# Kernel tuning notes

Hardware: AMD Instinct MI355X
Metric: run time of the kernel (lower is better)

Reference implementation:

```python
import jax, jax.numpy as jnp
import numpy as np

T, HW, C = 64, 24, 1024
MID = 256
WIN = 2  # 'video' forward_type -> 2x2 windows


def setup_inputs() -> dict:
    key = jax.random.key(0)
    k1, k2, k3, k4, k5 = jax.random.split(key, 5)
    return {
        "image_features": jax.random.normal(k1, (T, HW * HW, C), dtype=jnp.float32),
        "Wq": jax.random.normal(k2, (C, MID), dtype=jnp.float32) * 0.02,
        "bq": jax.random.normal(k3, (MID,), dtype=jnp.float32) * 0.02,
        "Wk": jax.random.normal(k4, (C, MID), dtype=jnp.float32) * 0.02,
        "bk": jax.random.normal(k5, (MID,), dtype=jnp.float32) * 0.02,
    }


def reference(image_features, Wq, bq, Wk, bk):
    # forward_type == 'video': 2x2 windowed attention over pooled patches
    t, n, c = image_features.shape
    H = W = int(np.sqrt(n))
    h2, w2 = H // WIN, W // WIN
    # [T, H, W, C] -> [T, h2, 2, w2, 2, C] -> [T, h2, w2, 2, 2, C] -> [T, P, 4, C]
    x = image_features.reshape(t, h2, WIN, w2, WIN, c)
    windows = x.transpose(0, 1, 3, 2, 4, 5).reshape(t, h2 * w2, WIN * WIN, c)
    # avg_pool2d(2,2) == mean over each 2x2 window
    pooled = windows.mean(axis=2)  # [T, P, C]
    q = pooled @ Wq + bq           # [T, P, MID]
    k = windows @ Wk + bk          # [T, P, 4, MID]
    scale = 1.0 / jnp.sqrt(jnp.float32(MID))
    attn = jnp.einsum("tpd,tpwd->tpw", q, k) * scale  # [T, P, 4]
    attn = jnp.nan_to_num(attn)
    attn = jax.nn.softmax(attn, axis=-1)
    attn_feat = jnp.einsum("tpw,tpwc->tpc", attn, windows)  # softmax-weighted value avg
    # query dim has size 1, so .mean(1) in torch is identity here
    return pooled + attn_feat  # [T, P, C]; new_image_size = (h2, w2) is static
```

## Files before the change

kernel.cpp:

```cpp
#include <hip/hip_runtime.h>

#define T_ 64
#define P_ 144
#define NPAIR 9216
#define C_ 1024
#define MID_ 256

typedef __attribute__((ext_vector_type(4))) float f32x4;
typedef __attribute__((ext_vector_type(8))) __bf16 bf16x8;
typedef __attribute__((ext_vector_type(4))) __bf16 bf16x4;

__device__ __forceinline__ void async_copy16(const void* g, void* l) {
  __builtin_amdgcn_global_load_lds(
      (const __attribute__((address_space(1))) unsigned int*)g,
      (__attribute__((address_space(3))) unsigned int*)l, 16, 0, 0);
}

__global__ __launch_bounds__(256) void pool_prep_kernel(
    const float* __restrict__ img, const float* __restrict__ Wq,
    const float* __restrict__ Wk, __bf16* __restrict__ poolb,
    __bf16* __restrict__ Wqt, __bf16* __restrict__ Wkb) {
  const int bid = blockIdx.x;
  const int tid = threadIdx.x;
  if (bid < NPAIR) {
    const int t = bid / P_;
    const int p = bid - t * P_;
    const int wy = p / 12, wx = p - wy * 12;
    const int c = tid * 4;
    const float* base = img + ((size_t)t * 576 + 48 * wy + 2 * wx) * C_;
    f32x4 s = *(const f32x4*)(base + c);
    s += *(const f32x4*)(base + (size_t)1 * C_ + c);
    s += *(const f32x4*)(base + (size_t)24 * C_ + c);
    s += *(const f32x4*)(base + (size_t)25 * C_ + c);
    s *= 0.25f;
    bf16x4 pv;
#pragma unroll
    for (int j = 0; j < 4; ++j) pv[j] = (__bf16)s[j];
    *(bf16x4*)(poolb + (size_t)bid * C_ + c) = pv;
  } else if (bid < NPAIR + 64) {
    const int b = bid - NPAIR;
    const int ct = b >> 3, dt = b & 7;
    __shared__ float tile[128][33];
    const int r = tid >> 3;
    const int c4 = (tid & 7) * 4;
#pragma unroll
    for (int s = 0; s < 4; ++s) {
      const int row = r + s * 32;
      const f32x4 v =
          *(const f32x4*)(Wq + (size_t)(ct * 128 + row) * MID_ + dt * 32 + c4);
      tile[row][c4 + 0] = v[0]; tile[row][c4 + 1] = v[1];
      tile[row][c4 + 2] = v[2]; tile[row][c4 + 3] = v[3];
    }
    __syncthreads();
    const int dd = tid >> 5;
    const int cc4 = (tid & 31) * 4;
#pragma unroll
    for (int s = 0; s < 4; ++s) {
      const int d = dd + s * 8;
      bf16x4 o;
#pragma unroll
      for (int j = 0; j < 4; ++j) o[j] = (__bf16)tile[cc4 + j][d];
      *(bf16x4*)(Wqt + (size_t)(dt * 32 + d) * C_ + ct * 128 + cc4) = o;
    }
  } else {
    const int b = bid - NPAIR - 64;
    const float* src = Wk + (size_t)b * 8192;
    __bf16* dst = Wkb + (size_t)b * 8192;
#pragma unroll
    for (int s = 0; s < 8; ++s) {
      const f32x4 v = *(const f32x4*)(src + tid * 4 + s * 1024);
      bf16x4 o;
#pragma unroll
      for (int j = 0; j < 4; ++j) o[j] = (__bf16)v[j];
      *(bf16x4*)(dst + tid * 4 + s * 1024) = o;
    }
  }
}

__global__ __launch_bounds__(256) void gemm_q_kernel(
    const __bf16* __restrict__ A, const __bf16* __restrict__ Bt,
    const float* __restrict__ bias, __bf16* __restrict__ Q) {
  __shared__ __align__(16) __bf16 As[64 * 32];
  __shared__ __align__(16) __bf16 Bs[128 * 32];
  const int bid = blockIdx.x;
  const int mt = bid >> 1, nt = bid & 1;
  const int tid = threadIdx.x;
  const int lane = tid & 63;
  const int wv = tid >> 6;
  const int quad = lane >> 4, lr = lane & 15;
  const int wm = wv >> 1, wn = wv & 1;

  const int r0 = tid >> 2, p0 = tid & 3;
  const int wvb = (tid & ~63) * 16;
  const __bf16* ga0 = A + ((size_t)mt * 64 + r0) * (size_t)C_ + p0 * 8;
  const __bf16* gb0 = Bt + ((size_t)nt * 128 + r0) * (size_t)C_ + p0 * 8;
  const __bf16* gb1 = gb0 + (size_t)64 * C_;
  char* AsB0 = (char*)As + wvb;
  char* BsB0 = (char*)Bs + wvb;
  char* BsB1 = (char*)Bs + 4096 + wvb;

  f32x4 acc[2][4] = {};

  for (int it = 0; it < 32; ++it) {
    async_copy16(ga0, AsB0);
    async_copy16(gb0, BsB0);
    async_copy16(gb1, BsB1);
    ga0 += 32; gb0 += 32; gb1 += 32;
    __syncthreads();
    bf16x8 a[2], b[4];
    const bf16x8* Ap = (const bf16x8*)As;
    const bf16x8* Bp = (const bf16x8*)Bs;
#pragma unroll
    for (int i = 0; i < 2; ++i) a[i] = Ap[(wm * 32 + i * 16 + lr) * 4 + quad];
#pragma unroll
    for (int i = 0; i < 4; ++i) b[i] = Bp[(wn * 64 + i * 16 + lr) * 4 + quad];
#pragma unroll
    for (int mi = 0; mi < 2; ++mi)
#pragma unroll
      for (int ni = 0; ni < 4; ++ni)
        acc[mi][ni] = __builtin_amdgcn_mfma_f32_16x16x32_bf16(
            a[mi], b[ni], acc[mi][ni], 0, 0, 0);
    __syncthreads();
  }

  const int colb = nt * 128 + wn * 64;
  const int rowb = mt * 64 + wm * 32 + quad * 4;
#pragma unroll
  for (int ni = 0; ni < 4; ++ni) {
    const int col = colb + ni * 16 + lr;
    const float bv = bias[col];
#pragma unroll
    for (int mi = 0; mi < 2; ++mi) {
      const int row = rowb + mi * 16;
#pragma unroll
      for (int r = 0; r < 4; ++r)
        Q[(size_t)(row + r) * MID_ + col] = (__bf16)(acc[mi][ni][r] + bv);
    }
  }
}

__global__ __launch_bounds__(256) void gemm_u_kernel(
    const __bf16* __restrict__ A, const __bf16* __restrict__ Bt,
    __bf16* __restrict__ U) {
  __shared__ __align__(16) __bf16 As[128 * 32];
  __shared__ __align__(16) __bf16 Bs[128 * 32];
  const int bid = blockIdx.x;
  const int mt = bid >> 3, nt = bid & 7;
  const int tid = threadIdx.x;
  const int lane = tid & 63;
  const int wv = tid >> 6;
  const int quad = lane >> 4, lr = lane & 15;
  const int wm = wv >> 1, wn = wv & 1;

  const int r0 = tid >> 2, p0 = tid & 3;
  const int wvb = (tid & ~63) * 16;
  const __bf16* ga0 = A + ((size_t)mt * 128 + r0) * (size_t)MID_ + p0 * 8;
  const __bf16* ga1 = ga0 + (size_t)64 * MID_;
  const __bf16* gb0 = Bt + ((size_t)nt * 128 + r0) * (size_t)MID_ + p0 * 8;
  const __bf16* gb1 = gb0 + (size_t)64 * MID_;
  char* AsB0 = (char*)As + wvb;
  char* AsB1 = (char*)As + 4096 + wvb;
  char* BsB0 = (char*)Bs + wvb;
  char* BsB1 = (char*)Bs + 4096 + wvb;

  f32x4 acc[4][4] = {};

  for (int it = 0; it < 8; ++it) {
    async_copy16(ga0, AsB0);
    async_copy16(ga1, AsB1);
    async_copy16(gb0, BsB0);
    async_copy16(gb1, BsB1);
    ga0 += 32; ga1 += 32; gb0 += 32; gb1 += 32;
    __syncthreads();
    bf16x8 a[4], b[4];
    const bf16x8* Ap = (const bf16x8*)As;
    const bf16x8* Bp = (const bf16x8*)Bs;
#pragma unroll
    for (int i = 0; i < 4; ++i) {
      a[i] = Ap[(wm * 64 + i * 16 + lr) * 4 + quad];
      b[i] = Bp[(wn * 64 + i * 16 + lr) * 4 + quad];
    }
#pragma unroll
    for (int mi = 0; mi < 4; ++mi)
#pragma unroll
      for (int ni = 0; ni < 4; ++ni)
        acc[mi][ni] = __builtin_amdgcn_mfma_f32_16x16x32_bf16(
            a[mi], b[ni], acc[mi][ni], 0, 0, 0);
    __syncthreads();
  }

  const int colb = nt * 128 + wn * 64;
  const int rowb = mt * 128 + wm * 64 + quad * 4;
#pragma unroll
  for (int ni = 0; ni < 4; ++ni) {
    const int col = colb + ni * 16 + lr;
#pragma unroll
    for (int mi = 0; mi < 4; ++mi) {
      const int row = rowb + mi * 16;
#pragma unroll
      for (int r = 0; r < 4; ++r)
        U[(size_t)(row + r) * C_ + col] = (__bf16)acc[mi][ni][r];
    }
  }
}

__global__ __launch_bounds__(256) void attn_out_kernel(
    const __bf16* __restrict__ U, const float* __restrict__ img,
    float* __restrict__ out) {
  const int tid = threadIdx.x;
  const int wv = tid >> 6, lane = tid & 63;
  const int pair = blockIdx.x * 4 + wv;
  const int t = pair / P_;
  const int pp = pair - t * P_;
  const int wy = pp / 12, wx = pp - wy * 12;
  const float* base = img + ((size_t)t * 576 + 48 * wy + 2 * wx) * C_;

  f32x4 v0[4], v1[4], v2[4], v3[4], u4[4];
  float pd0 = 0.f, pd1 = 0.f, pd2 = 0.f, pd3 = 0.f;
#pragma unroll
  for (int ch = 0; ch < 4; ++ch) {
    const int c = lane * 4 + ch * 256;
    v0[ch] = *(const f32x4*)(base + c);
    v1[ch] = *(const f32x4*)(base + (size_t)1 * C_ + c);
    v2[ch] = *(const f32x4*)(base + (size_t)24 * C_ + c);
    v3[ch] = *(const f32x4*)(base + (size_t)25 * C_ + c);
    const bf16x4 ub = *(const bf16x4*)(U + (size_t)pair * C_ + c);
#pragma unroll
    for (int j = 0; j < 4; ++j) u4[ch][j] = (float)ub[j];
#pragma unroll
    for (int j = 0; j < 4; ++j) {
      pd0 += u4[ch][j] * v0[ch][j];
      pd1 += u4[ch][j] * v1[ch][j];
      pd2 += u4[ch][j] * v2[ch][j];
      pd3 += u4[ch][j] * v3[ch][j];
    }
  }
#pragma unroll
  for (int m = 32; m >= 1; m >>= 1) {
    pd0 += __shfl_xor(pd0, m);
    pd1 += __shfl_xor(pd1, m);
    pd2 += __shfl_xor(pd2, m);
    pd3 += __shfl_xor(pd3, m);
  }
  const float l0 = pd0 * 0.0625f, l1 = pd1 * 0.0625f;
  const float l2 = pd2 * 0.0625f, l3 = pd3 * 0.0625f;
  const float mx = fmaxf(fmaxf(l0, l1), fmaxf(l2, l3));
  const float e0 = __expf(l0 - mx), e1 = __expf(l1 - mx);
  const float e2 = __expf(l2 - mx), e3 = __expf(l3 - mx);
  const float inv = 1.f / (e0 + e1 + e2 + e3);
  const float a0 = e0 * inv + 0.25f, a1 = e1 * inv + 0.25f;
  const float a2 = e2 * inv + 0.25f, a3 = e3 * inv + 0.25f;
  float* op = out + (size_t)pair * C_;
#pragma unroll
  for (int ch = 0; ch < 4; ++ch) {
    const int c = lane * 4 + ch * 256;
    f32x4 o = a0 * v0[ch] + a1 * v1[ch] + a2 * v2[ch] + a3 * v3[ch];
    *(f32x4*)(op + c) = o;
  }
}

extern "C" void kernel_launch(void* const* d_in, const int* in_sizes, int n_in,
                              void* d_out, int out_size, void* d_ws,
                              size_t ws_size, hipStream_t stream) {
  const float* img = (const float*)d_in[0];
  const float* Wq = (const float*)d_in[1];
  const float* bq = (const float*)d_in[2];
  const float* Wk = (const float*)d_in[3];
  const float* bk = (const float*)d_in[4];
  (void)bk;
  float* out = (float*)d_out;

  char* ws = (char*)d_ws;
  __bf16* poolb = (__bf16*)ws;
  __bf16* Wqt = (__bf16*)(ws + 18874368);
  __bf16* Wkb = (__bf16*)(ws + 19398656);
  __bf16* Qb  = (__bf16*)(ws + 19922944);
  __bf16* U   = (__bf16*)(ws + 24641536);

  pool_prep_kernel<<<NPAIR + 96, 256, 0, stream>>>(img, Wq, Wk, poolb, Wqt, Wkb);
  gemm_q_kernel<<<288, 256, 0, stream>>>(poolb, Wqt, bq, Qb);
  gemm_u_kernel<<<576, 256, 0, stream>>>(Qb, Wkb, U);
  attn_out_kernel<<<NPAIR / 4, 256, 0, stream>>>(U, img, out);
}
```

Baseline: 285.4 us.

## Fuse 2x2 pooling into the Q-projection GEMM, drop pooled bf16 buffer

```diff
diff --git a/kernel.cpp b/kernel.cpp
--- a/kernel.cpp
+++ b/kernel.cpp
@@ -16,30 +16,13 @@
       (__attribute__((address_space(3))) unsigned int*)l, 16, 0, 0);
 }
 
-__global__ __launch_bounds__(256) void pool_prep_kernel(
-    const float* __restrict__ img, const float* __restrict__ Wq,
-    const float* __restrict__ Wk, __bf16* __restrict__ poolb,
+__global__ __launch_bounds__(256) void prep_kernel(
+    const float* __restrict__ Wq, const float* __restrict__ Wk,
     __bf16* __restrict__ Wqt, __bf16* __restrict__ Wkb) {
   const int bid = blockIdx.x;
   const int tid = threadIdx.x;
-  if (bid < NPAIR) {
-    const int t = bid / P_;
-    const int p = bid - t * P_;
-    const int wy = p / 12, wx = p - wy * 12;
-    const int c = tid * 4;
-    const float* base = img + ((size_t)t * 576 + 48 * wy + 2 * wx) * C_;
-    f32x4 s = *(const f32x4*)(base + c);
-    s += *(const f32x4*)(base + (size_t)1 * C_ + c);
-    s += *(const f32x4*)(base + (size_t)24 * C_ + c);
-    s += *(const f32x4*)(base + (size_t)25 * C_ + c);
-    s *= 0.25f;
-    bf16x4 pv;
-#pragma unroll
-    for (int j = 0; j < 4; ++j) pv[j] = (__bf16)s[j];
-    *(bf16x4*)(poolb + (size_t)bid * C_ + c) = pv;
-  } else if (bid < NPAIR + 64) {
-    const int b = bid - NPAIR;
-    const int ct = b >> 3, dt = b & 7;
+  if (bid < 64) {
+    const int ct = bid >> 3, dt = bid & 7;
     __shared__ float tile[128][33];
     const int r = tid >> 3;
     const int c4 = (tid & 7) * 4;
@@ -63,7 +46,7 @@
       *(bf16x4*)(Wqt + (size_t)(dt * 32 + d) * C_ + ct * 128 + cc4) = o;
     }
   } else {
-    const int b = bid - NPAIR - 64;
+    const int b = bid - 64;
     const float* src = Wk + (size_t)b * 8192;
     __bf16* dst = Wkb + (size_t)b * 8192;
 #pragma unroll
@@ -77,64 +60,74 @@
   }
 }
 
-__global__ __launch_bounds__(256) void gemm_q_kernel(
-    const __bf16* __restrict__ A, const __bf16* __restrict__ Bt,
-    const float* __restrict__ bias, __bf16* __restrict__ Q) {
-  __shared__ __align__(16) __bf16 As[64 * 32];
-  __shared__ __align__(16) __bf16 Bs[128 * 32];
+__global__ __launch_bounds__(256) void gemm_qp_kernel(
+    const float* __restrict__ img, const __bf16* __restrict__ Wqt,
+    const float* __restrict__ bq, __bf16* __restrict__ Q) {
+  __shared__ __align__(16) __bf16 As[16 * 32];
+  __shared__ __align__(16) __bf16 hs[256 * 32];
+  __shared__ float bqs[MID_];
+  const int tid = threadIdx.x;
   const int bid = blockIdx.x;
-  const int mt = bid >> 1, nt = bid & 1;
-  const int tid = threadIdx.x;
   const int lane = tid & 63;
   const int wv = tid >> 6;
   const int quad = lane >> 4, lr = lane & 15;
-  const int wm = wv >> 1, wn = wv & 1;
-
-  const int r0 = tid >> 2, p0 = tid & 3;
-  const int wvb = (tid & ~63) * 16;
-  const __bf16* ga0 = A + ((size_t)mt * 64 + r0) * (size_t)C_ + p0 * 8;
-  const __bf16* gb0 = Bt + ((size_t)nt * 128 + r0) * (size_t)C_ + p0 * 8;
-  const __bf16* gb1 = gb0 + (size_t)64 * C_;
-  char* AsB0 = (char*)As + wvb;
-  char* BsB0 = (char*)Bs + wvb;
-  char* BsB1 = (char*)Bs + 4096 + wvb;
-
-  f32x4 acc[2][4] = {};
+
+  if (tid < MID_) bqs[tid] = bq[tid];
+
+  const int pair = tid >> 3;
+  const int chg = (tid & 7) * 4;
+  const int gp = bid * 16 + pair;
+  const int t = gp / P_;
+  const int pp = gp - t * P_;
+  const int wy = pp / 12, wx = pp - wy * 12;
+  const float* abase = img + ((size_t)t * 576 + 48 * wy + 2 * wx) * C_ + chg;
+  __bf16* adst = As + pair * 32 + chg;
+
+  const int tb = tid - 128;
+  const __bf16* gb = Wqt + (size_t)((tb * 2) >> 1) * 0;
+  char* hdst = (char*)hs + tb * 16;
+
+  f32x4 acc[4] = {};
 
   for (int it = 0; it < 32; ++it) {
-    async_copy16(ga0, AsB0);
-    async_copy16(gb0, BsB0);
-    async_copy16(gb1, BsB1);
-    ga0 += 32; gb0 += 32; gb1 += 32;
-    __syncthreads();
-    bf16x8 a[2], b[4];
-    const bf16x8* Ap = (const bf16x8*)As;
-    const bf16x8* Bp = (const bf16x8*)Bs;
-#pragma unroll
-    for (int i = 0; i < 2; ++i) a[i] = Ap[(wm * 32 + i * 16 + lr) * 4 + quad];
-#pragma unroll
-    for (int i = 0; i < 4; ++i) b[i] = Bp[(wn * 64 + i * 16 + lr) * 4 + quad];
-#pragma unroll
-    for (int mi = 0; mi < 2; ++mi)
-#pragma unroll
-      for (int ni = 0; ni < 4; ++ni)
-        acc[mi][ni] = __builtin_amdgcn_mfma_f32_16x16x32_bf16(
-            a[mi], b[ni], acc[mi][ni], 0, 0, 0);
-    __syncthreads();
-  }
-
-  const int colb = nt * 128 + wn * 64;
-  const int rowb = mt * 64 + wm * 32 + quad * 4;
-#pragma unroll
-  for (int ni = 0; ni < 4; ++ni) {
-    const int col = colb + ni * 16 + lr;
-    const float bv = bias[col];
-#pragma unroll
-    for (int mi = 0; mi < 2; ++mi) {
-      const int row = rowb + mi * 16;
-#pragma unroll
-      for (int r = 0; r < 4; ++r)
-        Q[(size_t)(row + r) * MID_ + col] = (__bf16)(acc[mi][ni][r] + bv);
+    if (tid < 128) {
+      const float* src = abase + it * 32;
+      f32x4 sm = *(const f32x4*)(src);
+      sm += *(const f32x4*)(src + C_);
+      sm += *(const f32x4*)(src + 24 * C_);
+      sm += *(const f32x4*)(src + 25 * C_);
+      sm *= 0.25f;
+      bf16x4 pv;
+#pragma unroll
+      for (int q = 0; q < 4; ++q) pv[q] = (__bf16)sm[q];
+      *(bf16x4*)(adst) = pv;
+    } else {
+#pragma unroll
+      for (int i = 0; i < 8; ++i) {
+        const int u = tb + i * 128;
+        const __bf16* src = Wqt + (size_t)(u >> 2) * C_ + (u & 3) * 8 + it * 32;
+        async_copy16(src, hdst + i * 2048);
+      }
+    }
+    __syncthreads();
+    const bf16x8 a = *(const bf16x8*)(As + lr * 32 + quad * 8);
+#pragma unroll
+    for (int j = 0; j < 4; ++j) {
+      const bf16x8 b = *(const bf16x8*)(hs + (wv * 64 + j * 16 + lr) * 32 + quad * 8);
+      acc[j] = __builtin_amdgcn_mfma_f32_16x16x32_bf16(a, b, acc[j], 0, 0, 0);
+    }
+    __syncthreads();
+  }
+  (void)gb;
+
+#pragma unroll
+  for (int j = 0; j < 4; ++j) {
+    const int col = wv * 64 + j * 16 + lr;
+    const float bv = bqs[col];
+#pragma unroll
+    for (int r = 0; r < 4; ++r) {
+      const int row = quad * 4 + r;
+      Q[((size_t)bid * 16 + row) * MID_ + col] = (__bf16)(acc[j][r] + bv);
     }
   }
 }
@@ -271,14 +264,13 @@
   float* out = (float*)d_out;
 
   char* ws = (char*)d_ws;
-  __bf16* poolb = (__bf16*)ws;
-  __bf16* Wqt = (__bf16*)(ws + 18874368);
-  __bf16* Wkb = (__bf16*)(ws + 19398656);
-  __bf16* Qb  = (__bf16*)(ws + 19922944);
-  __bf16* U   = (__bf16*)(ws + 24641536);
-
-  pool_prep_kernel<<<NPAIR + 96, 256, 0, stream>>>(img, Wq, Wk, poolb, Wqt, Wkb);
-  gemm_q_kernel<<<288, 256, 0, stream>>>(poolb, Wqt, bq, Qb);
+  __bf16* Wqt = (__bf16*)ws;
+  __bf16* Wkb = (__bf16*)(ws + 524288);
+  __bf16* Qb  = (__bf16*)(ws + 1048576);
+  __bf16* U   = (__bf16*)(ws + 5767168);
+
+  prep_kernel<<<96, 256, 0, stream>>>(Wq, Wk, Wqt, Wkb);
+  gemm_qp_kernel<<<576, 256, 0, stream>>>(img, Wqt, bq, Qb);
   gemm_u_kernel<<<576, 256, 0, stream>>>(Qb, Wkb, U);
   attn_out_kernel<<<NPAIR / 4, 256, 0, stream>>>(U, img, out);
 }
```

New measurement: 313.9 us. 10.0% more time.
